# Kernel optimization log

Measured on AMD Instinct MI355X. Metric: run time of the kernel, lower is better.

## Reference

```python
import jax, jax.numpy as jnp
import numpy as np

TIME_STEP = 3
TOPK = 84


def setup_inputs() -> dict:
    key = jax.random.key(0)
    kx, _ = jax.random.split(key)
    x = jax.random.uniform(kx, (8, 2, 352, 2048), dtype=jnp.float32)
    w = jnp.ones((), dtype=jnp.float32)
    return {"x": x, "w": w}


def reference(x, w):
    b, c, f, l = x.shape
    emb = c * TIME_STEP
    last = x[:, :, :, -1:]  # (b,c,f,1) last frame, used as right-padding
    # shift i: x[..., i:] padded on the right with i copies of the last frame
    parts = [
        x if i == 0 else jnp.concatenate(
            [x[:, :, :, i:], jnp.broadcast_to(last, (b, c, f, i))], axis=-1)
        for i in range(TIME_STEP)
    ]
    shifted = jnp.concatenate(parts, axis=1)            # (b, emb, f, l)
    shifted = shifted.transpose(0, 2, 3, 1).reshape(b, f * l, emb)  # (b, N, emb)

    query = shifted.mean(axis=1, keepdims=True)         # (b, 1, emb)
    scores = jnp.einsum('bqe,bne->bqn', query, shifted)[:, 0]  # (b, N)

    topk_scores, topk_idx = jax.lax.top_k(scores, TOPK)  # (b, K)
    vals = jnp.take_along_axis(shifted, topk_idx[:, :, None], axis=1)  # (b, K, emb)
    attn = jax.nn.softmax(topk_scores, axis=-1)          # (b, K)

    out = jnp.einsum('bk,bke->be', attn, vals) * w + query[:, 0] * (0.5 - w)  # (b, emb)
    return out.reshape(b, c, 1, TIME_STEP)
```

## Files before the change

kernel.cpp:

```cpp
#include <hip/hip_runtime.h>
#include <math.h>

#define LL 2048
#define FF 352
#define BATCH 8
#define TOPK 84
#define FPB 4
#define BPB (FF / FPB)
#define NBINS 8192
#define BINSCALE 1024.0f
#define SUBBINS 8192
#define CAP 32768
#define BCAP 2048
#define FINCAP 512
#define RPB 8
#define NPART (NROWS / RPB)
#define NROWS (BATCH * 2 * FF)
#define FL (FF * LL)
#define CNTSTRIDE 64

#define OFF_Q 64
#define OFF_CNT 128
#define OFF_PART 1024
#define OFF_CS 32768
#define OFF_CI 294912

__device__ __forceinline__ int coarse_bin(float sv) {
    int bin = (int)(fmaxf(sv, 0.f) * BINSCALE);
    return bin > NBINS - 1 ? NBINS - 1 : bin;
}
__device__ __forceinline__ int fine_bin(float sv, int t) {
    float f = fmaxf(sv, 0.f) * BINSCALE - (float)t;
    int s = (int)(f * (float)SUBBINS);
    s = s < 0 ? 0 : s;
    return s > SUBBINS - 1 ? SUBBINS - 1 : s;
}

template<int NB>
__device__ __forceinline__ void find_thresh(const unsigned int* hist, int K,
                                            int tid, int lane, int wid,
                                            int* wtot, int* sres) {
    constexpr int CW = NB / 256;
    int csum = 0;
    #pragma unroll
    for (int k = 0; k < CW; ++k) csum += (int)hist[tid * CW + ((k + tid) & (CW - 1))];
    int sfx = csum;
    #pragma unroll
    for (int d = 1; d < 64; d <<= 1) {
        int o = __shfl_down(sfx, d);
        if (lane + d < 64) sfx += o;
    }
    if (lane == 0) wtot[wid] = sfx;
    __syncthreads();
    int hi = 0;
    #pragma unroll
    for (int w2 = 0; w2 < 4; ++w2) if (w2 > wid) hi += wtot[w2];
    int SC = sfx + hi;
    int SCn = SC - csum;
    if (SC >= K && SCn < K) { sres[0] = tid; sres[1] = SCn; }
    __syncthreads();
    int cstar = sres[0], aboveC = sres[1];
    if (tid < 64) {
        int hv = (tid < CW) ? (int)hist[cstar * CW + tid] : 0;
        int s2 = hv;
        #pragma unroll
        for (int d = 1; d < CW; d <<= 1) {
            int o = __shfl_down(s2, d);
            if (tid + d < 64) s2 += o;
        }
        int ge = aboveC + s2;
        int gt = ge - hv;
        if (tid < CW && ge >= K && gt < K) { sres[2] = cstar * CW + tid; sres[3] = gt; }
    }
    __syncthreads();
}

__global__ __launch_bounds__(256) void k_rowsum(const float* __restrict__ x,
                                                float* __restrict__ ws,
                                                int* __restrict__ wsi) {
    int g = blockIdx.x;
    int tid = threadIdx.x;
    if (g == 0 && tid < 8) wsi[OFF_CNT + tid * CNTSTRIDE] = 0;
    int bc = g / 44, sub = g % 44;
    int rr = tid >> 5, c = tid & 31;
    const float4* rp = (const float4*)(x + (size_t)(bc * FF + sub * RPB + rr) * LL);
    float s = 0.f, x0c = 0.f, x1c = 0.f, xlc = 0.f;
    #pragma unroll
    for (int k = 0; k < 16; ++k) {
        float4 v = rp[c + (k << 5)];
        s += v.x + v.y + v.z + v.w;
        if (k == 0 && c == 0) { x0c = v.x; x1c = v.y; }
        if (k == 15 && c == 31) xlc = v.w;
    }
    int lane = tid & 63, wid = tid >> 6;
    for (int off = 32; off; off >>= 1) {
        s += __shfl_down(s, off);
        x0c += __shfl_down(x0c, off);
        x1c += __shfl_down(x1c, off);
        xlc += __shfl_down(xlc, off);
    }
    __shared__ float4 red[4];
    if (lane == 0) red[wid] = make_float4(s, x0c, x1c, xlc);
    __syncthreads();
    if (tid == 0) {
        float4 p = make_float4(0.f, 0.f, 0.f, 0.f);
        for (int w2 = 0; w2 < 4; ++w2) {
            p.x += red[w2].x; p.y += red[w2].y; p.z += red[w2].z; p.w += red[w2].w;
        }
        ((float4*)(ws + OFF_PART))[g] = p;
    }
}

__global__ __launch_bounds__(256, 4) void k_score(const float* __restrict__ x,
                                                  float* __restrict__ ws,
                                                  int* __restrict__ wsi) {
    __shared__ unsigned int hist[NBINS];
    __shared__ float4 red0[4], red1[4];
    __shared__ float sq[6];
    __shared__ int wtot[4], sres[4];
    __shared__ int lcnt, lbase;
    int tid = threadIdx.x;
    int b = blockIdx.x / BPB, blk = blockIdx.x % BPB;
    int fb = blk * FPB;
    int lane = tid & 63, wid = tid >> 6;

    for (int k = 0; k < NBINS / 256; ++k) hist[tid + (k << 8)] = 0u;
    if (tid == 0) lcnt = 0;

    float4 acc0 = {0.f, 0.f, 0.f, 0.f}, acc1 = {0.f, 0.f, 0.f, 0.f};
    if (tid < 88) {
        int ch = tid / 44, sb = tid % 44;
        float4 p = ((const float4*)(ws + OFF_PART))[(2 * b + ch) * 44 + sb];
        if (ch == 0) acc0 = p; else acc1 = p;
    }
    for (int off = 32; off; off >>= 1) {
        acc0.x += __shfl_down(acc0.x, off); acc0.y += __shfl_down(acc0.y, off);
        acc0.z += __shfl_down(acc0.z, off); acc0.w += __shfl_down(acc0.w, off);
        acc1.x += __shfl_down(acc1.x, off); acc1.y += __shfl_down(acc1.y, off);
        acc1.z += __shfl_down(acc1.z, off); acc1.w += __shfl_down(acc1.w, off);
    }
    if (lane == 0) { red0[wid] = acc0; red1[wid] = acc1; }
    __syncthreads();
    if (tid == 0) {
        float A0 = 0, B0 = 0, C0 = 0, D0 = 0, A1 = 0, B1 = 0, C1 = 0, D1 = 0;
        for (int w2 = 0; w2 < 4; ++w2) {
            A0 += red0[w2].x; B0 += red0[w2].y; C0 += red0[w2].z; D0 += red0[w2].w;
            A1 += red1[w2].x; B1 += red1[w2].y; C1 += red1[w2].z; D1 += red1[w2].w;
        }
        const float inv = 1.f / (float)FL;
        sq[0] = A0 * inv;
        sq[1] = A1 * inv;
        sq[2] = (A0 - B0 + D0) * inv;
        sq[3] = (A1 - B1 + D1) * inv;
        sq[4] = (A0 - B0 - C0 + 2.f * D0) * inv;
        sq[5] = (A1 - B1 - C1 + 2.f * D1) * inv;
        if (blk == 0) for (int e = 0; e < 6; ++e) ws[OFF_Q + b * 6 + e] = sq[e];
    }
    __syncthreads();
    float q0 = sq[0], q1 = sq[1], q2 = sq[2], q3 = sq[3], q4 = sq[4], q5 = sq[5];

    const float* r0p[FPB];
    const float* r1p[FPB];
    #pragma unroll
    for (int fr = 0; fr < FPB; ++fr) {
        r0p[fr] = x + ((size_t)(b * 2 + 0) * FF + fb + fr) * LL;
        r1p[fr] = x + ((size_t)(b * 2 + 1) * FF + fb + fr) * LL;
    }

    float pa4[FPB][2], pa5[FPB][2], pb4[FPB][2], pb5[FPB][2];
    if (lane == 63) {
        #pragma unroll
        for (int fr = 0; fr < FPB; ++fr) {
            #pragma unroll
            for (int h = 0; h < 2; ++h) {
                int l0 = (h << 10) + tid * 4;
                if (l0 != LL - 4) {
                    pa4[fr][h] = r0p[fr][l0 + 4]; pa5[fr][h] = r0p[fr][l0 + 5];
                    pb4[fr][h] = r1p[fr][l0 + 4]; pb5[fr][h] = r1p[fr][l0 + 5];
                }
            }
        }
    }

    float4 sreg[FPB][2];
    float4 u = *(const float4*)(r0p[0] + tid * 4);
    float4 v = *(const float4*)(r1p[0] + tid * 4);
    #pragma unroll
    for (int fr = 0; fr < FPB; ++fr) {
        #pragma unroll
        for (int h = 0; h < 2; ++h) {
            int l0 = (h << 10) + tid * 4;
            int nfr = (h == 1) ? fr + 1 : fr;
            int nh = (h == 1) ? 0 : 1;
            float4 un, vn;
            bool have_next = (nfr < FPB);
            if (have_next) {
                int ln = (nh << 10) + tid * 4;
                un = *(const float4*)(r0p[nfr] + ln);
                vn = *(const float4*)(r1p[nfr] + ln);
            }
            float a4 = __shfl_down(u.x, 1), a5 = __shfl_down(u.y, 1);
            float b4 = __shfl_down(v.x, 1), b5 = __shfl_down(v.y, 1);
            if (lane == 63) {
                if (l0 == LL - 4) { a4 = u.w; a5 = u.w; b4 = v.w; b5 = v.w; }
                else { a4 = pa4[fr][h]; a5 = pa5[fr][h];
                       b4 = pb4[fr][h]; b5 = pb5[fr][h]; }
            }
            float4 s;
            s.x = q0 * u.x + q1 * v.x + q2 * u.y + q3 * v.y + q4 * u.z + q5 * v.z;
            s.y = q0 * u.y + q1 * v.y + q2 * u.z + q3 * v.z + q4 * u.w + q5 * v.w;
            s.z = q0 * u.z + q1 * v.z + q2 * u.w + q3 * v.w + q4 * a4 + q5 * b4;
            s.w = q0 * u.w + q1 * v.w + q2 * a4 + q3 * b4 + q4 * a5 + q5 * b5;
            sreg[fr][h] = s;
            #pragma unroll
            for (int j = 0; j < 4; ++j) {
                float sv = j == 0 ? s.x : (j == 1 ? s.y : (j == 2 ? s.z : s.w));
                atomicAdd(&hist[coarse_bin(sv)], 1u);
            }
            if (have_next) { u = un; v = vn; }
        }
    }
    __syncthreads();

    find_thresh<NBINS>(hist, TOPK, tid, lane, wid, wtot, sres);
    int t = sres[2];

    unsigned int kmask = 0u;
    #pragma unroll
    for (int fr = 0; fr < FPB; ++fr) {
        #pragma unroll
        for (int h = 0; h < 2; ++h) {
            float4 s = sreg[fr][h];
            #pragma unroll
            for (int j = 0; j < 4; ++j) {
                float sv = j == 0 ? s.x : (j == 1 ? s.y : (j == 2 ? s.z : s.w));
                if (coarse_bin(sv) >= t) kmask |= 1u << ((fr << 3) + (h << 2) + j);
            }
        }
    }
    int cnt = __popc(kmask);
    int myoff = 0;
    if (cnt) myoff = atomicAdd(&lcnt, cnt);
    __syncthreads();
    if (tid == 0) lbase = atomicAdd(&wsi[OFF_CNT + b * CNTSTRIDE], lcnt);
    __syncthreads();
    int pos = lbase + myoff;
    #pragma unroll
    for (int fr = 0; fr < FPB; ++fr) {
        #pragma unroll
        for (int h = 0; h < 2; ++h) {
            float4 s = sreg[fr][h];
            int l0 = (h << 10) + tid * 4;
            int nb = (fb + fr) * LL + l0;
            #pragma unroll
            for (int j = 0; j < 4; ++j) {
                if (kmask & (1u << ((fr << 3) + (h << 2) + j))) {
                    float sv = j == 0 ? s.x : (j == 1 ? s.y : (j == 2 ? s.z : s.w));
                    if (pos < CAP) {
                        ws[OFF_CS + b * CAP + pos] = sv;
                        wsi[OFF_CI + b * CAP + pos] = nb + j;
                    }
                    ++pos;
                }
            }
        }
    }
}

__global__ __launch_bounds__(256) void k_final(const float* __restrict__ x,
                                               const float* __restrict__ wv,
                                               const float* __restrict__ ws,
                                               const int* __restrict__ wsi,
                                               float* __restrict__ out) {
    __shared__ unsigned int hist[NBINS];
    __shared__ float bls[BCAP];
    __shared__ int bli[BCAP];
    __shared__ float fins[FINCAP];
    __shared__ int fini[FINCAP];
    __shared__ int wtot[4], sres[4];
    __shared__ int bcnt, c2s;
    __shared__ float redm[4];
    __shared__ float den;
    __shared__ float accsh[8];
    int tid = threadIdx.x;
    int b = blockIdx.x;
    int lane = tid & 63, wid = tid >> 6;

    int C = wsi[OFF_CNT + b * CNTSTRIDE];
    if (C > CAP) C = CAP;
    const float* gcs = ws + OFF_CS + b * CAP;
    const int* gci = wsi + OFF_CI + b * CAP;

    for (int k = 0; k < NBINS / 256; ++k) hist[tid + (k << 8)] = 0u;
    if (tid == 0) bcnt = 0;
    __syncthreads();
    for (int base = 0; base < C; base += 4096) {
        int j0 = base + tid * 4;
        float4 s0 = *(const float4*)(gcs + j0);
        float4 s1 = *(const float4*)(gcs + j0 + 1024);
        float4 s2 = *(const float4*)(gcs + j0 + 2048);
        float4 s3 = *(const float4*)(gcs + j0 + 3072);
        #pragma unroll
        for (int q = 0; q < 4; ++q) {
            float4 sq4 = q == 0 ? s0 : (q == 1 ? s1 : (q == 2 ? s2 : s3));
            int jq = j0 + q * 1024;
            #pragma unroll
            for (int j = 0; j < 4; ++j) {
                if (jq + j < C) {
                    float sv = j == 0 ? sq4.x : (j == 1 ? sq4.y : (j == 2 ? sq4.z : sq4.w));
                    atomicAdd(&hist[coarse_bin(sv)], 1u);
                }
            }
        }
    }
    __syncthreads();
    find_thresh<NBINS>(hist, TOPK, tid, lane, wid, wtot, sres);
    int t = sres[2];

    for (int base = 0; base < C; base += 4096) {
        int j0 = base + tid * 4;
        float4 s0 = *(const float4*)(gcs + j0);
        float4 s1 = *(const float4*)(gcs + j0 + 1024);
        float4 s2 = *(const float4*)(gcs + j0 + 2048);
        float4 s3 = *(const float4*)(gcs + j0 + 3072);
        int4 i0 = *(const int4*)(gci + j0);
        int4 i1 = *(const int4*)(gci + j0 + 1024);
        int4 i2 = *(const int4*)(gci + j0 + 2048);
        int4 i3 = *(const int4*)(gci + j0 + 3072);
        #pragma unroll
        for (int q = 0; q < 4; ++q) {
            float4 sq4 = q == 0 ? s0 : (q == 1 ? s1 : (q == 2 ? s2 : s3));
            int4 iq4 = q == 0 ? i0 : (q == 1 ? i1 : (q == 2 ? i2 : i3));
            int jq = j0 + q * 1024;
            #pragma unroll
            for (int j = 0; j < 4; ++j) {
                if (jq + j < C) {
                    float sv = j == 0 ? sq4.x : (j == 1 ? sq4.y : (j == 2 ? sq4.z : sq4.w));
                    int iv = j == 0 ? iq4.x : (j == 1 ? iq4.y : (j == 2 ? iq4.z : iq4.w));
                    if (coarse_bin(sv) >= t) {
                        int p = atomicAdd(&bcnt, 1);
                        if (p < BCAP) { bls[p] = sv; bli[p] = iv; }
                    }
                }
            }
        }
    }
    __syncthreads();
    int nb = bcnt < BCAP ? bcnt : BCAP;

    for (int k = 0; k < NBINS / 256; ++k) hist[tid + (k << 8)] = 0u;
    __syncthreads();
    for (int p = tid; p < nb; p += 256) {
        float sv = bls[p];
        int fk = coarse_bin(sv) > t ? SUBBINS - 1 : fine_bin(sv, t);
        atomicAdd(&hist[fk], 1u);
    }
    __syncthreads();
    find_thresh<NBINS>(hist, TOPK, tid, lane, wid, wtot, sres);
    int t2 = sres[2];
    if (tid == 0) c2s = 0;
    __syncthreads();
    for (int p = tid; p < nb; p += 256) {
        float sv = bls[p];
        int fk = coarse_bin(sv) > t ? SUBBINS - 1 : fine_bin(sv, t);
        if (fk >= t2) {
            int q = atomicAdd(&c2s, 1);
            if (q < FINCAP) { fins[q] = sv; fini[q] = bli[p]; }
        }
    }
    __syncthreads();
    int C2 = c2s < FINCAP ? c2s : FINCAP;

    if (tid < 8) accsh[tid] = 0.f;
    if (tid == 0) den = 0.f;
    __syncthreads();

    float m = -INFINITY;
    for (int p = tid; p < C2; p += 256) m = fmaxf(m, fins[p]);
    for (int off = 32; off; off >>= 1) m = fmaxf(m, __shfl_down(m, off));
    if (lane == 0) redm[wid] = m;
    __syncthreads();
    float smax = fmaxf(fmaxf(redm[0], redm[1]), fmaxf(redm[2], redm[3]));

    float g0 = 0.f, g1 = 0.f, g2 = 0.f, g3 = 0.f, g4 = 0.f, g5 = 0.f, dden = 0.f;
    for (int p = tid; p < C2; p += 256) {
        float s = fins[p];
        int idx = fini[p];
        int rank = 0;
        for (int j = 0; j < C2; ++j) {
            float sj = fins[j];
            int ij = fini[j];
            rank += (sj > s) || (sj == s && ij < idx);
        }
        if (rank < TOPK) {
            float pexp = expf(s - smax);
            dden += pexp;
            int f = idx >> 11, l = idx & (LL - 1);
            int l1 = l + 1 < LL ? l + 1 : LL - 1;
            int l2 = l + 2 < LL ? l + 2 : LL - 1;
            const float* r0 = x + ((size_t)(b * 2 + 0) * FF + f) * LL;
            const float* r1 = x + ((size_t)(b * 2 + 1) * FF + f) * LL;
            g0 += pexp * r0[l];
            g1 += pexp * r1[l];
            g2 += pexp * r0[l1];
            g3 += pexp * r1[l1];
            g4 += pexp * r0[l2];
            g5 += pexp * r1[l2];
        }
    }
    for (int off = 32; off; off >>= 1) {
        dden += __shfl_down(dden, off);
        g0 += __shfl_down(g0, off); g1 += __shfl_down(g1, off);
        g2 += __shfl_down(g2, off); g3 += __shfl_down(g3, off);
        g4 += __shfl_down(g4, off); g5 += __shfl_down(g5, off);
    }
    if (lane == 0) {
        atomicAdd(&den, dden);
        atomicAdd(&accsh[0], g0); atomicAdd(&accsh[1], g1);
        atomicAdd(&accsh[2], g2); atomicAdd(&accsh[3], g3);
        atomicAdd(&accsh[4], g4); atomicAdd(&accsh[5], g5);
    }
    __syncthreads();
    if (tid < 6) {
        float w = wv[0];
        float q = ws[OFF_Q + b * 6 + tid];
        out[b * 6 + tid] = (accsh[tid] / den) * w + q * (0.5f - w);
    }
}

extern "C" void kernel_launch(void* const* d_in, const int* in_sizes, int n_in,
                              void* d_out, int out_size, void* d_ws, size_t ws_size,
                              hipStream_t stream) {
    const float* x = (const float*)d_in[0];
    const float* w = (const float*)d_in[1];
    float* out = (float*)d_out;
    float* wsf = (float*)d_ws;
    int* wsi = (int*)d_ws;

    k_rowsum<<<NPART, 256, 0, stream>>>(x, wsf, wsi);
    k_score<<<BATCH * BPB, 256, 0, stream>>>(x, wsf, wsi);
    k_final<<<BATCH, 256, 0, stream>>>(x, w, wsf, wsi, out);
}
```

Before: 112.3 us.

## Give each wavefront its own frame row and private coarse histogram, removing block syncs

After: 127.3 us. 1.13x slower.

```diff
diff --git a/kernel.cpp b/kernel.cpp
--- a/kernel.cpp
+++ b/kernel.cpp
@@ -7,10 +7,12 @@
 #define TOPK 84
 #define FPB 4
 #define BPB (FF / FPB)
+#define WBINS 512
+#define WBINSCALE 64.0f
 #define NBINS 8192
 #define BINSCALE 1024.0f
 #define SUBBINS 8192
-#define CAP 32768
+#define CAP 65536
 #define BCAP 2048
 #define FINCAP 512
 #define RPB 8
@@ -23,8 +25,12 @@
 #define OFF_CNT 128
 #define OFF_PART 1024
 #define OFF_CS 32768
-#define OFF_CI 294912
-
+#define OFF_CI 557056
+
+__device__ __forceinline__ int wbin(float sv) {
+    int bin = (int)(fmaxf(sv, 0.f) * WBINSCALE);
+    return bin > WBINS - 1 ? WBINS - 1 : bin;
+}
 __device__ __forceinline__ int coarse_bin(float sv) {
     int bin = (int)(fmaxf(sv, 0.f) * BINSCALE);
     return bin > NBINS - 1 ? NBINS - 1 : bin;
@@ -111,157 +117,139 @@
     }
 }
 
-__global__ __launch_bounds__(256, 4) void k_score(const float* __restrict__ x,
-                                                  float* __restrict__ ws,
-                                                  int* __restrict__ wsi) {
-    __shared__ unsigned int hist[NBINS];
-    __shared__ float4 red0[4], red1[4];
-    __shared__ float sq[6];
-    __shared__ int wtot[4], sres[4];
-    __shared__ int lcnt, lbase;
+__global__ __launch_bounds__(256) void k_score(const float* __restrict__ x,
+                                               float* __restrict__ ws,
+                                               int* __restrict__ wsi) {
+    __shared__ unsigned int hist[FPB][WBINS];
     int tid = threadIdx.x;
     int b = blockIdx.x / BPB, blk = blockIdx.x % BPB;
-    int fb = blk * FPB;
-    int lane = tid & 63, wid = tid >> 6;
-
-    for (int k = 0; k < NBINS / 256; ++k) hist[tid + (k << 8)] = 0u;
-    if (tid == 0) lcnt = 0;
+    int lane = tid & 63, w = tid >> 6;
+    int f = blk * FPB + w;
+    unsigned int* whist = hist[w];
+
+    #pragma unroll
+    for (int j = 0; j < WBINS / 64; ++j) whist[lane + (j << 6)] = 0u;
 
     float4 acc0 = {0.f, 0.f, 0.f, 0.f}, acc1 = {0.f, 0.f, 0.f, 0.f};
-    if (tid < 88) {
-        int ch = tid / 44, sb = tid % 44;
-        float4 p = ((const float4*)(ws + OFF_PART))[(2 * b + ch) * 44 + sb];
-        if (ch == 0) acc0 = p; else acc1 = p;
-    }
-    for (int off = 32; off; off >>= 1) {
-        acc0.x += __shfl_down(acc0.x, off); acc0.y += __shfl_down(acc0.y, off);
-        acc0.z += __shfl_down(acc0.z, off); acc0.w += __shfl_down(acc0.w, off);
-        acc1.x += __shfl_down(acc1.x, off); acc1.y += __shfl_down(acc1.y, off);
-        acc1.z += __shfl_down(acc1.z, off); acc1.w += __shfl_down(acc1.w, off);
-    }
-    if (lane == 0) { red0[wid] = acc0; red1[wid] = acc1; }
-    __syncthreads();
-    if (tid == 0) {
-        float A0 = 0, B0 = 0, C0 = 0, D0 = 0, A1 = 0, B1 = 0, C1 = 0, D1 = 0;
-        for (int w2 = 0; w2 < 4; ++w2) {
-            A0 += red0[w2].x; B0 += red0[w2].y; C0 += red0[w2].z; D0 += red0[w2].w;
-            A1 += red1[w2].x; B1 += red1[w2].y; C1 += red1[w2].z; D1 += red1[w2].w;
-        }
-        const float inv = 1.f / (float)FL;
-        sq[0] = A0 * inv;
-        sq[1] = A1 * inv;
-        sq[2] = (A0 - B0 + D0) * inv;
-        sq[3] = (A1 - B1 + D1) * inv;
-        sq[4] = (A0 - B0 - C0 + 2.f * D0) * inv;
-        sq[5] = (A1 - B1 - C1 + 2.f * D1) * inv;
-        if (blk == 0) for (int e = 0; e < 6; ++e) ws[OFF_Q + b * 6 + e] = sq[e];
-    }
-    __syncthreads();
-    float q0 = sq[0], q1 = sq[1], q2 = sq[2], q3 = sq[3], q4 = sq[4], q5 = sq[5];
-
-    const float* r0p[FPB];
-    const float* r1p[FPB];
-    #pragma unroll
-    for (int fr = 0; fr < FPB; ++fr) {
-        r0p[fr] = x + ((size_t)(b * 2 + 0) * FF + fb + fr) * LL;
-        r1p[fr] = x + ((size_t)(b * 2 + 1) * FF + fb + fr) * LL;
-    }
-
-    float pa4[FPB][2], pa5[FPB][2], pb4[FPB][2], pb5[FPB][2];
-    if (lane == 63) {
+    if (lane < 44) {
+        const float4* part = (const float4*)(ws + OFF_PART);
+        acc0 = part[(2 * b + 0) * 44 + lane];
+        acc1 = part[(2 * b + 1) * 44 + lane];
+    }
+    #pragma unroll
+    for (int d = 1; d < 64; d <<= 1) {
+        acc0.x += __shfl_xor(acc0.x, d); acc0.y += __shfl_xor(acc0.y, d);
+        acc0.z += __shfl_xor(acc0.z, d); acc0.w += __shfl_xor(acc0.w, d);
+        acc1.x += __shfl_xor(acc1.x, d); acc1.y += __shfl_xor(acc1.y, d);
+        acc1.z += __shfl_xor(acc1.z, d); acc1.w += __shfl_xor(acc1.w, d);
+    }
+    const float inv = 1.f / (float)FL;
+    float q0 = acc0.x * inv;
+    float q1 = acc1.x * inv;
+    float q2 = (acc0.x - acc0.y + acc0.w) * inv;
+    float q3 = (acc1.x - acc1.y + acc1.w) * inv;
+    float q4 = (acc0.x - acc0.y - acc0.z + 2.f * acc0.w) * inv;
+    float q5 = (acc1.x - acc1.y - acc1.z + 2.f * acc1.w) * inv;
+    if (blk == 0 && w == 0 && lane == 0) {
+        ws[OFF_Q + b * 6 + 0] = q0; ws[OFF_Q + b * 6 + 1] = q1;
+        ws[OFF_Q + b * 6 + 2] = q2; ws[OFF_Q + b * 6 + 3] = q3;
+        ws[OFF_Q + b * 6 + 4] = q4; ws[OFF_Q + b * 6 + 5] = q5;
+    }
+
+    const float* r0 = x + ((size_t)(b * 2 + 0) * FF + f) * LL;
+    const float* r1 = x + ((size_t)(b * 2 + 1) * FF + f) * LL;
+    float4 sreg[8];
+    float4 u = *(const float4*)(r0 + lane * 4);
+    float4 v = *(const float4*)(r1 + lane * 4);
+    #pragma unroll
+    for (int k = 0; k < 8; ++k) {
+        float4 un, vn;
+        bool have_next = (k < 7);
+        if (have_next) {
+            int ln = ((k + 1) << 8) + lane * 4;
+            un = *(const float4*)(r0 + ln);
+            vn = *(const float4*)(r1 + ln);
+        }
+        float a4 = __shfl_down(u.x, 1), a5 = __shfl_down(u.y, 1);
+        float b4 = __shfl_down(v.x, 1), b5 = __shfl_down(v.y, 1);
+        if (have_next) {
+            float nxa4 = __shfl(un.x, 0), nxa5 = __shfl(un.y, 0);
+            float nxb4 = __shfl(vn.x, 0), nxb5 = __shfl(vn.y, 0);
+            if (lane == 63) { a4 = nxa4; a5 = nxa5; b4 = nxb4; b5 = nxb5; }
+        } else {
+            if (lane == 63) { a4 = u.w; a5 = u.w; b4 = v.w; b5 = v.w; }
+        }
+        float4 s;
+        s.x = q0 * u.x + q1 * v.x + q2 * u.y + q3 * v.y + q4 * u.z + q5 * v.z;
+        s.y = q0 * u.y + q1 * v.y + q2 * u.z + q3 * v.z + q4 * u.w + q5 * v.w;
+        s.z = q0 * u.z + q1 * v.z + q2 * u.w + q3 * v.w + q4 * a4 + q5 * b4;
+        s.w = q0 * u.w + q1 * v.w + q2 * a4 + q3 * b4 + q4 * a5 + q5 * b5;
+        sreg[k] = s;
+        atomicAdd(&whist[wbin(s.x)], 1u);
+        atomicAdd(&whist[wbin(s.y)], 1u);
+        atomicAdd(&whist[wbin(s.z)], 1u);
+        atomicAdd(&whist[wbin(s.w)], 1u);
+        if (have_next) { u = un; v = vn; }
+    }
+
+    int csum = 0;
+    #pragma unroll
+    for (int j = 0; j < 8; ++j) csum += (int)whist[(lane << 3) + ((j + lane) & 7)];
+    int sfx = csum;
+    #pragma unroll
+    for (int d = 1; d < 64; d <<= 1) {
+        int o = __shfl_down(sfx, d);
+        if (lane + d < 64) sfx += o;
+    }
+    int SCn = sfx - csum;
+    unsigned long long mask = __ballot(sfx >= TOPK && SCn < TOPK);
+    int cstar = __ffsll(mask) - 1;
+    int aboveC = __shfl(SCn, cstar);
+    int t = cstar << 3;
+    int cum = aboveC;
+    #pragma unroll
+    for (int jj = 7; jj >= 0; --jj) {
+        int hv = (int)whist[(cstar << 3) + jj];
+        cum += hv;
+        if (cum >= TOPK) { t = (cstar << 3) + jj; break; }
+    }
+
+    unsigned int kmask = 0u;
+    int cnt = 0;
+    #pragma unroll
+    for (int k = 0; k < 8; ++k) {
+        float4 s = sreg[k];
         #pragma unroll
-        for (int fr = 0; fr < FPB; ++fr) {
-            #pragma unroll
-            for (int h = 0; h < 2; ++h) {
-                int l0 = (h << 10) + tid * 4;
-                if (l0 != LL - 4) {
-                    pa4[fr][h] = r0p[fr][l0 + 4]; pa5[fr][h] = r0p[fr][l0 + 5];
-                    pb4[fr][h] = r1p[fr][l0 + 4]; pb5[fr][h] = r1p[fr][l0 + 5];
+        for (int j = 0; j < 4; ++j) {
+            float sv = j == 0 ? s.x : (j == 1 ? s.y : (j == 2 ? s.z : s.w));
+            if (wbin(sv) >= t) { kmask |= 1u << ((k << 2) + j); ++cnt; }
+        }
+    }
+    int inc = cnt;
+    #pragma unroll
+    for (int d = 1; d < 64; d <<= 1) {
+        int o = __shfl_up(inc, d);
+        if (lane >= d) inc += o;
+    }
+    int exc = inc - cnt;
+    int total = __shfl(inc, 63);
+    int base = 0;
+    if (lane == 0) base = atomicAdd(&wsi[OFF_CNT + b * CNTSTRIDE], total);
+    base = __shfl(base, 0);
+    int pos = base + exc;
+    #pragma unroll
+    for (int k = 0; k < 8; ++k) {
+        float4 s = sreg[k];
+        int nb = f * LL + (k << 8) + lane * 4;
+        #pragma unroll
+        for (int j = 0; j < 4; ++j) {
+            if (kmask & (1u << ((k << 2) + j))) {
+                float sv = j == 0 ? s.x : (j == 1 ? s.y : (j == 2 ? s.z : s.w));
+                if (pos < CAP) {
+                    ws[OFF_CS + b * CAP + pos] = sv;
+                    wsi[OFF_CI + b * CAP + pos] = nb + j;
                 }
-            }
-        }
-    }
-
-    float4 sreg[FPB][2];
-    float4 u = *(const float4*)(r0p[0] + tid * 4);
-    float4 v = *(const float4*)(r1p[0] + tid * 4);
-    #pragma unroll
-    for (int fr = 0; fr < FPB; ++fr) {
-        #pragma unroll
-        for (int h = 0; h < 2; ++h) {
-            int l0 = (h << 10) + tid * 4;
-            int nfr = (h == 1) ? fr + 1 : fr;
-            int nh = (h == 1) ? 0 : 1;
-            float4 un, vn;
-            bool have_next = (nfr < FPB);
-            if (have_next) {
-                int ln = (nh << 10) + tid * 4;
-                un = *(const float4*)(r0p[nfr] + ln);
-                vn = *(const float4*)(r1p[nfr] + ln);
-            }
-            float a4 = __shfl_down(u.x, 1), a5 = __shfl_down(u.y, 1);
-            float b4 = __shfl_down(v.x, 1), b5 = __shfl_down(v.y, 1);
-            if (lane == 63) {
-                if (l0 == LL - 4) { a4 = u.w; a5 = u.w; b4 = v.w; b5 = v.w; }
-                else { a4 = pa4[fr][h]; a5 = pa5[fr][h];
-                       b4 = pb4[fr][h]; b5 = pb5[fr][h]; }
-            }
-            float4 s;
-            s.x = q0 * u.x + q1 * v.x + q2 * u.y + q3 * v.y + q4 * u.z + q5 * v.z;
-            s.y = q0 * u.y + q1 * v.y + q2 * u.z + q3 * v.z + q4 * u.w + q5 * v.w;
-            s.z = q0 * u.z + q1 * v.z + q2 * u.w + q3 * v.w + q4 * a4 + q5 * b4;
-            s.w = q0 * u.w + q1 * v.w + q2 * a4 + q3 * b4 + q4 * a5 + q5 * b5;
-            sreg[fr][h] = s;
-            #pragma unroll
-            for (int j = 0; j < 4; ++j) {
-                float sv = j == 0 ? s.x : (j == 1 ? s.y : (j == 2 ? s.z : s.w));
-                atomicAdd(&hist[coarse_bin(sv)], 1u);
-            }
-            if (have_next) { u = un; v = vn; }
-        }
-    }
-    __syncthreads();
-
-    find_thresh<NBINS>(hist, TOPK, tid, lane, wid, wtot, sres);
-    int t = sres[2];
-
-    unsigned int kmask = 0u;
-    #pragma unroll
-    for (int fr = 0; fr < FPB; ++fr) {
-        #pragma unroll
-        for (int h = 0; h < 2; ++h) {
-            float4 s = sreg[fr][h];
-            #pragma unroll
-            for (int j = 0; j < 4; ++j) {
-                float sv = j == 0 ? s.x : (j == 1 ? s.y : (j == 2 ? s.z : s.w));
-                if (coarse_bin(sv) >= t) kmask |= 1u << ((fr << 3) + (h << 2) + j);
-            }
-        }
-    }
-    int cnt = __popc(kmask);
-    int myoff = 0;
-    if (cnt) myoff = atomicAdd(&lcnt, cnt);
-    __syncthreads();
-    if (tid == 0) lbase = atomicAdd(&wsi[OFF_CNT + b * CNTSTRIDE], lcnt);
-    __syncthreads();
-    int pos = lbase + myoff;
-    #pragma unroll
-    for (int fr = 0; fr < FPB; ++fr) {
-        #pragma unroll
-        for (int h = 0; h < 2; ++h) {
-            float4 s = sreg[fr][h];
-            int l0 = (h << 10) + tid * 4;
-            int nb = (fb + fr) * LL + l0;
-            #pragma unroll
-            for (int j = 0; j < 4; ++j) {
-                if (kmask & (1u << ((fr << 3) + (h << 2) + j))) {
-                    float sv = j == 0 ? s.x : (j == 1 ? s.y : (j == 2 ? s.z : s.w));
-                    if (pos < CAP) {
-                        ws[OFF_CS + b * CAP + pos] = sv;
-                        wsi[OFF_CI + b * CAP + pos] = nb + j;
-                    }
-                    ++pos;
-                }
+                ++pos;
             }
         }
     }
```
